# Kernel tuning notes

Measured on AMD Instinct MI355X. Metric: run time of the kernel, lower is better.

## Reference

```python
import jax, jax.numpy as jnp
import numpy as np

NUM_PQ = 8
TAU_Q = 1.0
EPS = 1e-12


def setup_inputs() -> dict:
    key = jax.random.key(0)
    k1, k2 = jax.random.split(key)
    z = jax.random.normal(k1, (8, 384, 32, 32), dtype=jnp.float32)
    # xavier_uniform bound for [2048, 384] is ~0.0497; approximate scale with normal init
    C = jax.random.normal(k2, (2048, 384), dtype=jnp.float32) * 0.05
    return {"z": z, "C": C, "it": 0}


def _soft_pq(z, C):
    b, c, h, w = z.shape
    K = NUM_PQ
    d = c // K
    # flatten spatial -> [N, K, d] sub-vectors (torch.split along channel == reshape)
    x = z.transpose(0, 2, 3, 1).reshape(-1, K, d)          # [N, K, d]
    cb = C.reshape(-1, K, d)                               # [M, K, d]
    x2 = jnp.sum(x * x, axis=-1)[:, :, None]               # [N, K, 1]
    c2 = jnp.sum(cb * cb, axis=-1).T[None, :, :]           # [1, K, M]
    xc = jnp.einsum('nkd,mkd->nkm', x, cb)                 # [N, K, M]
    dist = x2 + c2 - 2.0 * xc                              # [N, K, M]
    soft = jax.nn.softmax(-TAU_Q * dist, axis=-1)          # per-book softmax over M
    # soft assignment -> weighted codeword sum, concat over books
    Zq = jnp.einsum('nkm,mkd->nkd', soft, cb).reshape(-1, c)
    # JSD between first/second halves of the batch, per book, averaged over books
    N = soft.shape[0]
    p, q = soft[: N // 2], soft[N // 2 :]
    m = 0.5 * (p + q)
    logm = jnp.log(m + EPS)
    kl_pm = jnp.sum(p * (jnp.log(p + EPS) - logm), axis=-1)   # [N/2, K]
    kl_qm = jnp.sum(q * (jnp.log(q + EPS) - logm), axis=-1)
    # per-book JSD = mean over rows; sum over books / K == mean over both axes
    jsd = jnp.mean(0.5 * (kl_pm + kl_qm))
    z_quantized = Zq.reshape(b, h, w, c).transpose(0, 3, 1, 2)
    return z_quantized, jsd


def reference(z, C, it):
    z_quantized, jsd = _soft_pq(z, C)
    return z_quantized, jsd
```

## Files before the change

### kernel.cpp

```cpp
#include <hip/hip_runtime.h>


typedef __attribute__((ext_vector_type(8))) short short8;
typedef __attribute__((ext_vector_type(4))) float f32x4;

#define Z_BCH   (384*1024)
#define JSD_IDX 3145728
#define CS_TILE 9216
#define CT_TILE 6912
#define CT_OFF  (8*32*CS_TILE)

__device__ __forceinline__ f32x4 mfma32(short8 a, short8 b, f32x4 c) {
    return __builtin_amdgcn_mfma_f32_16x16x32_bf16(a, b, c, 0, 0, 0);
}
__device__ __forceinline__ unsigned short f2bf(float x) {
    unsigned u = __float_as_uint(x);
    u += 0x7FFF + ((u >> 16) & 1);
    return (unsigned short)(u >> 16);
}
__device__ __forceinline__ unsigned pk2bf(float a, float b) {
    return (unsigned)f2bf(a) | ((unsigned)f2bf(b) << 16);
}
__device__ __forceinline__ float bf2f(unsigned short h) {
    return __uint_as_float(((unsigned)h) << 16);
}

__global__ __launch_bounds__(256)
void pq_prep(const float* __restrict__ Cb, unsigned char* __restrict__ ws)
{
    const int tid = threadIdx.x;
    const int k   = blockIdx.x >> 5;
    const int t   = blockIdx.x & 31;
    const int sm  = tid & 63, p8 = tid >> 6;
    const int m   = t*64 + sm;

    unsigned short* csT = (unsigned short*)(ws + (size_t)(k*32 + t)*CS_TILE);
    unsigned short* ctT = (unsigned short*)(ws + CT_OFF + (size_t)(k*32 + t)*CT_TILE);

    const float4* crow = (const float4*)(Cb + (size_t)m*384 + k*48);
    float4 va = crow[p8*3+0], vb = crow[p8*3+1], vc = crow[p8*3+2];
    const int d0 = p8*12;
    *(uint2*)(csT + sm*72 + d0 + 0) = make_uint2(pk2bf(va.x,va.y), pk2bf(va.z,va.w));
    *(uint2*)(csT + sm*72 + d0 + 4) = make_uint2(pk2bf(vb.x,vb.y), pk2bf(vb.z,vb.w));
    *(uint2*)(csT + sm*72 + d0 + 8) = make_uint2(pk2bf(vc.x,vc.y), pk2bf(vc.z,vc.w));
    ctT[(d0+ 0)*72+sm] = f2bf(va.x);  ctT[(d0+ 1)*72+sm] = f2bf(va.y);
    ctT[(d0+ 2)*72+sm] = f2bf(va.z);  ctT[(d0+ 3)*72+sm] = f2bf(va.w);
    ctT[(d0+ 4)*72+sm] = f2bf(vb.x);  ctT[(d0+ 5)*72+sm] = f2bf(vb.y);
    ctT[(d0+ 6)*72+sm] = f2bf(vb.z);  ctT[(d0+ 7)*72+sm] = f2bf(vb.w);
    ctT[(d0+ 8)*72+sm] = f2bf(vc.x);  ctT[(d0+ 9)*72+sm] = f2bf(vc.y);
    ctT[(d0+10)*72+sm] = f2bf(vc.z);  ctT[(d0+11)*72+sm] = f2bf(vc.w);
    if (tid < 64) {
        const float4* cr2 = (const float4*)(Cb + (size_t)(t*64 + tid)*384 + k*48);
        float c2 = 0.f;
#pragma unroll
        for (int i = 0; i < 12; ++i) {
            float4 v = cr2[i];
            c2 += v.x*v.x + v.y*v.y + v.z*v.z + v.w*v.w;
        }
        float mh = -0.5f*c2;
        unsigned short hi = f2bf(mh);
        unsigned short lo = f2bf(mh - bf2f(hi));
        *(uint2*)(csT + tid*72 + 48) = make_uint2((unsigned)hi | ((unsigned)lo << 16), 0u);
        *(uint2*)(csT + tid*72 + 52) = make_uint2(0u, 0u);
        *(uint2*)(csT + tid*72 + 56) = make_uint2(0u, 0u);
        *(uint2*)(csT + tid*72 + 60) = make_uint2(0u, 0u);
    }
}

__global__ __launch_bounds__(512, 4)
void pq_pc(const float* __restrict__ Zin, const unsigned char* __restrict__ ws,
           float* __restrict__ Out)
{
    __shared__ __align__(16) unsigned char smem[54816];
    unsigned short* cs  = (unsigned short*)smem;
    unsigned short* ctb = (unsigned short*)(smem + 18432);
    unsigned short* xs  = (unsigned short*)smem;
    float* ztP  = (float*)(smem + 52736);
    float* ttP  = (float*)(smem + 52992);
    float* ztQ  = (float*)(smem + 53248);
    float* ttQ  = (float*)(smem + 53504);
    float* ipzP = (float*)(smem + 53760);
    float* ipzQ = (float*)(smem + 54016);
    float* entP = (float*)(smem + 54272);
    float* entQ = (float*)(smem + 54528);
    float* misc = (float*)(smem + 54784);
    float* obuf = (float*)smem;

    const int tid  = threadIdx.x;
    const int lane = tid & 63;
    const int wv   = tid >> 6;
    const int rg   = wv & 3;
    const int chw  = wv >> 2;
    const int lr   = lane & 15;
    const int lg   = lane >> 4;
    const int pg   = blockIdx.x & 63;
    const int k    = blockIdx.x >> 6;

    unsigned short* plds = (unsigned short*)(smem + 32256 + wv*2560);
    const unsigned char* csg = ws + (size_t)(k*32)*CS_TILE;
    const unsigned char* ctg = ws + CT_OFF + (size_t)(k*32)*CT_TILE;

    short8 av, on;
#pragma unroll
    for (int i = 0; i < 8; ++i) { av[i] = (short)f2bf((float)lr); on[i] = (short)0x3F80; }
    f32x4 zf4 = {0.f,0.f,0.f,0.f};
    f32x4 dmv = mfma32(av, on, zf4);
    f32x4 drv = mfma32(on, av, zf4);
    int mS[4], rS[4];
#pragma unroll
    for (int j = 0; j < 4; ++j) {
        mS[j] = ((int)(dmv[j]*0.03125f + 0.5f)) & 15;
        rS[j] = ((int)(drv[j]*0.03125f + 0.5f)) & 15;
    }
    const bool packOK = __all(mS[1] == mS[0]+1 && mS[2] == mS[0]+2 && mS[3] == mS[0]+3
                              && rS[1] == rS[0] && rS[2] == rS[0] && rS[3] == rS[0]);

    for (int i = tid; i < 4608; i += 512) ((unsigned*)smem)[i] = 0u;
    if (tid < 256) ((float*)(smem + 52736))[tid] = 0.f;
    __syncthreads();
    for (int i = tid; i < 6144; i += 512) {
        int row = i & 127, d = i >> 7;
        int n = pg*64 + (row & 63) + ((row & 64) ? 4096 : 0);
        xs[row*72 + d] = f2bf(Zin[(size_t)(n >> 10)*Z_BCH + (k*48 + d)*1024 + (n & 1023)]);
    }
    if (tid < 128) { xs[tid*72 + 48] = 0x3F80; xs[tid*72 + 49] = 0x3F80; }
    __syncthreads();
    short8 xf[2][2];
#pragma unroll
    for (int kh = 0; kh < 2; ++kh) {
        xf[0][kh] = *(const short8*)(xs + (rg*16 + lr)*72 + kh*32 + lg*8);
        xf[1][kh] = *(const short8*)(xs + (64 + rg*16 + lr)*72 + kh*32 + lg*8);
    }
    __syncthreads();

    uint4 r0, r1, r2;
#define LOADREG(t, doCT) do {                                                 \
        const unsigned char* _c = csg + (size_t)(t)*CS_TILE;                  \
        r0 = *(const uint4*)(_c + tid*16);                                    \
        if (tid < 64) r1 = *(const uint4*)(_c + 8192 + tid*16);               \
        if ((doCT) && tid < 432)                                              \
            r2 = *(const uint4*)(ctg + (size_t)(t)*CT_TILE + tid*16);         \
    } while (0)

#define SWRITE(b, doCT) do {                                                  \
        *(uint4*)(smem + (b)*CS_TILE + tid*16) = r0;                          \
        if (tid < 64) *(uint4*)(smem + (b)*CS_TILE + 8192 + tid*16) = r1;     \
        if ((doCT) && tid < 432)                                              \
            *(uint4*)(smem + 18432 + (b)*CT_TILE + tid*16) = r2;              \
    } while (0)

    float zp[4]={0,0,0,0}, tp[4]={0,0,0,0}, zq[4]={0,0,0,0}, tq[4]={0,0,0,0};

    LOADREG(0, false);
    SWRITE(0, false);
    LOADREG(1, false);
    __syncthreads();

#pragma unroll 1
    for (int t = 0; t < 32; ++t) {
        if (t < 31) SWRITE((t+1)&1, false);
        if (t < 30) LOADREG(t+2, false);
        const unsigned short* cst = cs + (t&1)*4608;
#pragma unroll
        for (int lmt = 0; lmt < 2; ++lmt) {
            const int mt = chw*2 + lmt;
            short8 a0 = *(const short8*)(cst + (mt*16 + lr)*72 + lg*8);
            short8 a1 = *(const short8*)(cst + (mt*16 + lr)*72 + 32 + lg*8);
            f32x4 accP = {0.f,0.f,0.f,0.f}, accQ = {0.f,0.f,0.f,0.f};
            accP = mfma32(a0, xf[0][0], accP);
            accP = mfma32(a1, xf[0][1], accP);
            accQ = mfma32(a0, xf[1][0], accQ);
            accQ = mfma32(a1, xf[1][1], accQ);
#pragma unroll
            for (int j = 0; j < 4; ++j) {
                float sp = 2.f*accP[j], sq = 2.f*accQ[j];
                float e1 = __expf(sp), e2 = __expf(sq);
                zp[j] += e1; tp[j] = fmaf(e1, sp, tp[j]);
                zq[j] += e2; tq[j] = fmaf(e2, sq, tq[j]);
            }
        }
        __syncthreads();
    }

#pragma unroll
    for (int j = 0; j < 4; ++j) {
        int r = rg*16 + rS[j];
        atomicAdd(ztP + r, zp[j]); atomicAdd(ttP + r, tp[j]);
        atomicAdd(ztQ + r, zq[j]); atomicAdd(ttQ + r, tq[j]);
    }
    __syncthreads();
    if (tid < 64) {
        float z1 = ztP[tid], t1 = ttP[tid];
        float z2 = ztQ[tid], t2 = ttQ[tid];
        float i1 = 1.f/z1, i2 = 1.f/z2;
        ipzP[tid] = i1; entP[tid] = t1*i1 - __logf(z1);
        ipzQ[tid] = i2; entQ[tid] = t2*i2 - __logf(z2);
    }
    __syncthreads();
    float izp_s[4], izq_s[4];
#pragma unroll
    for (int j = 0; j < 4; ++j) {
        izp_s[j] = ipzP[rg*16 + rS[j]];
        izq_s[j] = ipzQ[rg*16 + rS[j]];
    }

    f32x4 Op[3], Oq[3];
#pragma unroll
    for (int dt = 0; dt < 3; ++dt) { Op[dt] = (f32x4){0.f,0.f,0.f,0.f}; Oq[dt] = (f32x4){0.f,0.f,0.f,0.f}; }
    float cross = 0.f;

    LOADREG(0, true);
    SWRITE(0, true);
    LOADREG(1, true);
    __syncthreads();

#pragma unroll 1
    for (int t = 0; t < 32; ++t) {
        if (t < 31) SWRITE((t+1)&1, true);
        if (t < 30) LOADREG(t+2, true);
        const unsigned short* cst = cs + (t&1)*4608;
        const unsigned short* ctt = ctb + (t&1)*3456;
#pragma unroll
        for (int lmt = 0; lmt < 2; ++lmt) {
            const int mt = chw*2 + lmt;
            short8 a0 = *(const short8*)(cst + (mt*16 + lr)*72 + lg*8);
            short8 a1 = *(const short8*)(cst + (mt*16 + lr)*72 + 32 + lg*8);
            f32x4 accP = {0.f,0.f,0.f,0.f}, accQ = {0.f,0.f,0.f,0.f};
            accP = mfma32(a0, xf[0][0], accP);
            accP = mfma32(a1, xf[0][1], accP);
            accQ = mfma32(a0, xf[1][0], accQ);
            accQ = mfma32(a1, xf[1][1], accQ);
            float e1a[4], e2a[4];
#pragma unroll
            for (int j = 0; j < 4; ++j) {
                float e1 = __expf(2.f*accP[j]);
                float e2 = __expf(2.f*accQ[j]);
                e1a[j] = e1; e2a[j] = e2;
                float p = e1*izp_s[j], q = e2*izq_s[j];
                float ss = p + q;
                cross = fmaf(ss, __logf(fmaf(0.5f, ss, 1e-12f)), cross);
            }
            if (packOK) {
                *(uint2*)(plds + rS[0]*40        + lmt*16 + mS[0]) =
                    make_uint2(pk2bf(e1a[0], e1a[1]), pk2bf(e1a[2], e1a[3]));
                *(uint2*)(plds + (16 + rS[0])*40 + lmt*16 + mS[0]) =
                    make_uint2(pk2bf(e2a[0], e2a[1]), pk2bf(e2a[2], e2a[3]));
            } else {
#pragma unroll
                for (int j = 0; j < 4; ++j) {
                    plds[rS[j]*40        + lmt*16 + mS[j]] = f2bf(e1a[j]);
                    plds[(16 + rS[j])*40 + lmt*16 + mS[j]] = f2bf(e2a[j]);
                }
            }
        }
        {
            short8 pA = *(const short8*)(plds + lr*40        + lg*8);
            short8 qA = *(const short8*)(plds + (16 + lr)*40 + lg*8);
#pragma unroll
            for (int dt = 0; dt < 3; ++dt) {
                short8 cB = *(const short8*)(ctt + (dt*16 + lr)*72 + chw*32 + lg*8);
                Op[dt] = mfma32(pA, cB, Op[dt]);
                Oq[dt] = mfma32(qA, cB, Oq[dt]);
            }
        }
        __syncthreads();
    }

#pragma unroll
    for (int off = 1; off < 64; off <<= 1) cross += __shfl_xor(cross, off);
    if (lane == 0) misc[wv] = cross;

    if (chw == 1) {
#pragma unroll
        for (int dt = 0; dt < 3; ++dt)
#pragma unroll
            for (int j = 0; j < 4; ++j) {
                obuf[(rg*32 +      mS[j])*48 + dt*16 + rS[j]] = Op[dt][j];
                obuf[(rg*32 + 16 + mS[j])*48 + dt*16 + rS[j]] = Oq[dt][j];
            }
    }
    __syncthreads();

    if (tid == 0) {
        float es = 0.f;
        for (int r = 0; r < 64; ++r) es += entP[r] + entQ[r];
        float cr = 0.f;
        for (int w = 0; w < 8; ++w) cr += misc[w];
        atomicAdd(Out + JSD_IDX, (es - cr) * (0.5f/32768.f));
    }

    if (chw == 0) {
#pragma unroll
        for (int dt = 0; dt < 3; ++dt)
#pragma unroll
            for (int j = 0; j < 4; ++j) {
                int xr = mS[j];
                int np = pg*64 + rg*16 + xr;
                int nq = np + 4096;
                int chc = k*48 + dt*16 + rS[j];
                float vP = (Op[dt][j] + obuf[(rg*32 +      xr)*48 + dt*16 + rS[j]]) * ipzP[rg*16 + xr];
                float vQ = (Oq[dt][j] + obuf[(rg*32 + 16 + xr)*48 + dt*16 + rS[j]]) * ipzQ[rg*16 + xr];
                Out[(size_t)(np >> 10)*Z_BCH + (size_t)chc*1024 + (np & 1023)] = vP;
                Out[(size_t)(nq >> 10)*Z_BCH + (size_t)chc*1024 + (nq & 1023)] = vQ;
            }
    }
}

extern "C" void kernel_launch(void* const* d_in, const int* in_sizes, int n_in,
                              void* d_out, int out_size, void* d_ws, size_t ws_size,
                              hipStream_t stream)
{
    const float* z = (const float*)d_in[0];
    const float* C = (const float*)d_in[1];
    float* out = (float*)d_out;

    hipMemsetAsync(out + JSD_IDX, 0, sizeof(float), stream);

    pq_prep<<<dim3(256), dim3(256), 0, stream>>>(C, (unsigned char*)d_ws);
    pq_pc<<<dim3(512), dim3(512), 0, stream>>>(z, (const unsigned char*)d_ws, out);
}
```

Measured before the change: 146.6 us.

## Split fused PQ kernel into stats and output passes over halved codebook ranges

The single fused kernel is split into two kernels, pq_stats and pq_out, and each block now covers half of the codebook tiles. This doubles the grid from 512 to 1024 blocks for more parallelism. Row partition sums are combined through global atomics into a workspace, and the output is accumulated with atomicAdd, which requires zeroing the whole output buffer beforehand. The exponentials switch to exp2f/log2f with prescaled constants, and the codeword-transpose tile is read straight from global memory instead of being staged in LDS. In exchange it adds an extra launch, two memsets, recomputation of the x fragments and distances, and many float atomics on the output.

```diff
diff --git a/kernel.cpp b/kernel.cpp
--- a/kernel.cpp
+++ b/kernel.cpp
@@ -8,7 +8,11 @@
 #define JSD_IDX 3145728
 #define CS_TILE 9216
 #define CT_TILE 6912
-#define CT_OFF  (8*32*CS_TILE)
+#define CT_OFF  2359296
+#define ZS_OFF  4128768
+#define TS_OFF  (ZS_OFF + 262144)
+#define KC      2.8853900817779268f
+#define LN2     0.6931471805599453f
 
 __device__ __forceinline__ f32x4 mfma32(short8 a, short8 b, f32x4 c) {
     return __builtin_amdgcn_mfma_f32_16x16x32_bf16(a, b, c, 0, 0, 0);
@@ -67,100 +71,92 @@
     }
 }
 
-__global__ __launch_bounds__(512, 4)
-void pq_pc(const float* __restrict__ Zin, const unsigned char* __restrict__ ws,
-           float* __restrict__ Out)
-{
-    __shared__ __align__(16) unsigned char smem[54816];
-    unsigned short* cs  = (unsigned short*)smem;
-    unsigned short* ctb = (unsigned short*)(smem + 18432);
-    unsigned short* xs  = (unsigned short*)smem;
-    float* ztP  = (float*)(smem + 52736);
-    float* ttP  = (float*)(smem + 52992);
-    float* ztQ  = (float*)(smem + 53248);
-    float* ttQ  = (float*)(smem + 53504);
-    float* ipzP = (float*)(smem + 53760);
-    float* ipzQ = (float*)(smem + 54016);
-    float* entP = (float*)(smem + 54272);
-    float* entQ = (float*)(smem + 54528);
-    float* misc = (float*)(smem + 54784);
-    float* obuf = (float*)smem;
-
-    const int tid  = threadIdx.x;
-    const int lane = tid & 63;
-    const int wv   = tid >> 6;
-    const int rg   = wv & 3;
-    const int chw  = wv >> 2;
-    const int lr   = lane & 15;
-    const int lg   = lane >> 4;
-    const int pg   = blockIdx.x & 63;
-    const int k    = blockIdx.x >> 6;
-
-    unsigned short* plds = (unsigned short*)(smem + 32256 + wv*2560);
-    const unsigned char* csg = ws + (size_t)(k*32)*CS_TILE;
-    const unsigned char* ctg = ws + CT_OFF + (size_t)(k*32)*CT_TILE;
-
-    short8 av, on;
-#pragma unroll
-    for (int i = 0; i < 8; ++i) { av[i] = (short)f2bf((float)lr); on[i] = (short)0x3F80; }
-    f32x4 zf4 = {0.f,0.f,0.f,0.f};
-    f32x4 dmv = mfma32(av, on, zf4);
-    f32x4 drv = mfma32(on, av, zf4);
-    int mS[4], rS[4];
-#pragma unroll
-    for (int j = 0; j < 4; ++j) {
-        mS[j] = ((int)(dmv[j]*0.03125f + 0.5f)) & 15;
-        rS[j] = ((int)(drv[j]*0.03125f + 0.5f)) & 15;
-    }
-    const bool packOK = __all(mS[1] == mS[0]+1 && mS[2] == mS[0]+2 && mS[3] == mS[0]+3
-                              && rS[1] == rS[0] && rS[2] == rS[0] && rS[3] == rS[0]);
-
-    for (int i = tid; i < 4608; i += 512) ((unsigned*)smem)[i] = 0u;
-    if (tid < 256) ((float*)(smem + 52736))[tid] = 0.f;
-    __syncthreads();
-    for (int i = tid; i < 6144; i += 512) {
-        int row = i & 127, d = i >> 7;
-        int n = pg*64 + (row & 63) + ((row & 64) ? 4096 : 0);
-        xs[row*72 + d] = f2bf(Zin[(size_t)(n >> 10)*Z_BCH + (k*48 + d)*1024 + (n & 1023)]);
-    }
-    if (tid < 128) { xs[tid*72 + 48] = 0x3F80; xs[tid*72 + 49] = 0x3F80; }
-    __syncthreads();
-    short8 xf[2][2];
-#pragma unroll
-    for (int kh = 0; kh < 2; ++kh) {
-        xf[0][kh] = *(const short8*)(xs + (rg*16 + lr)*72 + kh*32 + lg*8);
-        xf[1][kh] = *(const short8*)(xs + (64 + rg*16 + lr)*72 + kh*32 + lg*8);
-    }
-    __syncthreads();
-
-    uint4 r0, r1, r2;
-#define LOADREG(t, doCT) do {                                                 \
+#define PQ_DECODE                                                             \
+    const int tid  = threadIdx.x;                                             \
+    const int lane = tid & 63;                                                \
+    const int wv   = tid >> 6;                                                \
+    const int rg   = wv & 3;                                                  \
+    const int chw  = wv >> 2;                                                 \
+    const int lr   = lane & 15;                                               \
+    const int lg   = lane >> 4;                                               \
+    const int pg   = blockIdx.x & 63;                                         \
+    const int half = (blockIdx.x >> 6) & 1;                                   \
+    const int k    = blockIdx.x >> 7;                                         \
+    const int t0   = half*16;
+
+#define PQ_PROBES                                                             \
+    short8 av, on;                                                            \
+    _Pragma("unroll")                                                         \
+    for (int i = 0; i < 8; ++i) { av[i] = (short)f2bf((float)lr); on[i] = (short)0x3F80; } \
+    f32x4 zf4 = {0.f,0.f,0.f,0.f};                                            \
+    f32x4 dmv = mfma32(av, on, zf4);                                          \
+    f32x4 drv = mfma32(on, av, zf4);                                          \
+    int mS[4], rS[4];                                                         \
+    _Pragma("unroll")                                                         \
+    for (int j = 0; j < 4; ++j) {                                             \
+        mS[j] = ((int)(dmv[j]*0.03125f + 0.5f)) & 15;                         \
+        rS[j] = ((int)(drv[j]*0.03125f + 0.5f)) & 15;                         \
+    }
+
+#define PQ_XFRAGS(Zin)                                                        \
+    for (int i = tid; i < 6144; i += 512) {                                   \
+        int row = i & 127, d = i >> 7;                                        \
+        int n = pg*64 + (row & 63) + ((row & 64) ? 4096 : 0);                 \
+        xs[row*72 + d] = f2bf(Zin[(size_t)(n >> 10)*Z_BCH + (k*48 + d)*1024 + (n & 1023)]); \
+    }                                                                         \
+    if (tid < 128) { xs[tid*72 + 48] = 0x3F80; xs[tid*72 + 49] = 0x3F80; }    \
+    __syncthreads();                                                          \
+    short8 xf[2][2];                                                          \
+    _Pragma("unroll")                                                         \
+    for (int kh = 0; kh < 2; ++kh) {                                          \
+        xf[0][kh] = *(const short8*)(xs + (rg*16 + lr)*72 + kh*32 + lg*8);    \
+        xf[1][kh] = *(const short8*)(xs + (64 + rg*16 + lr)*72 + kh*32 + lg*8); \
+    }                                                                         \
+    __syncthreads();
+
+#define LOADREG(t) do {                                                       \
         const unsigned char* _c = csg + (size_t)(t)*CS_TILE;                  \
         r0 = *(const uint4*)(_c + tid*16);                                    \
         if (tid < 64) r1 = *(const uint4*)(_c + 8192 + tid*16);               \
-        if ((doCT) && tid < 432)                                              \
-            r2 = *(const uint4*)(ctg + (size_t)(t)*CT_TILE + tid*16);         \
     } while (0)
-
-#define SWRITE(b, doCT) do {                                                  \
+#define SWRITE(b) do {                                                        \
         *(uint4*)(smem + (b)*CS_TILE + tid*16) = r0;                          \
         if (tid < 64) *(uint4*)(smem + (b)*CS_TILE + 8192 + tid*16) = r1;     \
-        if ((doCT) && tid < 432)                                              \
-            *(uint4*)(smem + 18432 + (b)*CT_TILE + tid*16) = r2;              \
     } while (0)
 
+__global__ __launch_bounds__(512, 8)
+void pq_stats(const float* __restrict__ Zin, const unsigned char* __restrict__ ws,
+              float* __restrict__ wsZ, float* __restrict__ wsT)
+{
+    __shared__ __align__(16) unsigned char smem[19456];
+    unsigned short* xs = (unsigned short*)smem;
+    float* ztP = (float*)(smem + 18432);
+    float* ttP = (float*)(smem + 18688);
+    float* ztQ = (float*)(smem + 18944);
+    float* ttQ = (float*)(smem + 19200);
+
+    PQ_DECODE
+    PQ_PROBES
+    const unsigned char* csg = ws + (size_t)(k*32)*CS_TILE;
+
+    for (int i = tid; i < 4608; i += 512) ((unsigned*)smem)[i] = 0u;
+    if (tid < 256) ((float*)(smem + 18432))[tid] = 0.f;
+    __syncthreads();
+    PQ_XFRAGS(Zin)
+
+    uint4 r0, r1;
     float zp[4]={0,0,0,0}, tp[4]={0,0,0,0}, zq[4]={0,0,0,0}, tq[4]={0,0,0,0};
 
-    LOADREG(0, false);
-    SWRITE(0, false);
-    LOADREG(1, false);
+    LOADREG(t0);
+    SWRITE(0);
+    LOADREG(t0+1);
     __syncthreads();
 
 #pragma unroll 1
-    for (int t = 0; t < 32; ++t) {
-        if (t < 31) SWRITE((t+1)&1, false);
-        if (t < 30) LOADREG(t+2, false);
-        const unsigned short* cst = cs + (t&1)*4608;
+    for (int t = 0; t < 16; ++t) {
+        if (t < 15) SWRITE((t+1)&1);
+        if (t < 14) LOADREG(t0+t+2);
+        const unsigned short* cst = (const unsigned short*)(smem + (t&1)*CS_TILE);
 #pragma unroll
         for (int lmt = 0; lmt < 2; ++lmt) {
             const int mt = chw*2 + lmt;
@@ -173,10 +169,10 @@
             accQ = mfma32(a1, xf[1][1], accQ);
 #pragma unroll
             for (int j = 0; j < 4; ++j) {
-                float sp = 2.f*accP[j], sq = 2.f*accQ[j];
-                float e1 = __expf(sp), e2 = __expf(sq);
-                zp[j] += e1; tp[j] = fmaf(e1, sp, tp[j]);
-                zq[j] += e2; tq[j] = fmaf(e2, sq, tq[j]);
+                float s2p = accP[j]*KC, s2q = accQ[j]*KC;
+                float e1 = exp2f(s2p), e2 = exp2f(s2q);
+                zp[j] += e1; tp[j] = fmaf(e1, s2p, tp[j]);
+                zq[j] += e2; tq[j] = fmaf(e2, s2q, tq[j]);
             }
         }
         __syncthreads();
@@ -189,37 +185,75 @@
         atomicAdd(ztQ + r, zq[j]); atomicAdd(ttQ + r, tq[j]);
     }
     __syncthreads();
-    if (tid < 64) {
-        float z1 = ztP[tid], t1 = ttP[tid];
-        float z2 = ztQ[tid], t2 = ttQ[tid];
-        float i1 = 1.f/z1, i2 = 1.f/z2;
-        ipzP[tid] = i1; entP[tid] = t1*i1 - __logf(z1);
-        ipzQ[tid] = i2; entQ[tid] = t2*i2 - __logf(z2);
+    if (tid < 128) {
+        int r = tid & 63;
+        int n = pg*64 + r + ((tid & 64) ? 4096 : 0);
+        float zv = (tid < 64) ? ztP[r] : ztQ[r];
+        float tv = (tid < 64) ? ttP[r] : ttQ[r];
+        atomicAdd(wsZ + (k << 13) + n, zv);
+        atomicAdd(wsT + (k << 13) + n, tv);
+    }
+}
+
+__global__ __launch_bounds__(512, 6)
+void pq_out(const float* __restrict__ Zin, const unsigned char* __restrict__ ws,
+            const float* __restrict__ wsZ, const float* __restrict__ wsT,
+            float* __restrict__ Out)
+{
+    __shared__ __align__(16) unsigned char smem[39968];
+    unsigned short* xs = (unsigned short*)smem;
+    float* ipz  = (float*)(smem + 38912);
+    float* ent  = (float*)(smem + 39424);
+    float* misc = (float*)(smem + 39936);
+    float* obuf = (float*)smem;
+
+    PQ_DECODE
+    PQ_PROBES
+    const bool packOK = __all(mS[1] == mS[0]+1 && mS[2] == mS[0]+2 && mS[3] == mS[0]+3
+                              && rS[1] == rS[0] && rS[2] == rS[0] && rS[3] == rS[0]);
+    const unsigned char* csg = ws + (size_t)(k*32)*CS_TILE;
+    const unsigned char* ctg = ws + CT_OFF + (size_t)(k*32)*CT_TILE;
+    unsigned short* plds = (unsigned short*)(smem + 18432 + wv*2560);
+
+    for (int i = tid; i < 4608; i += 512) ((unsigned*)smem)[i] = 0u;
+    __syncthreads();
+    PQ_XFRAGS(Zin)
+    if (tid < 128) {
+        int n = pg*64 + (tid & 63) + ((tid & 64) ? 4096 : 0);
+        float Zr = wsZ[(k << 13) + n];
+        float Tr = wsT[(k << 13) + n];
+        float iz = 1.f / Zr;
+        ipz[tid] = iz;
+        ent[tid] = LN2*(Tr*iz) - __logf(Zr);
     }
     __syncthreads();
     float izp_s[4], izq_s[4];
 #pragma unroll
     for (int j = 0; j < 4; ++j) {
-        izp_s[j] = ipzP[rg*16 + rS[j]];
-        izq_s[j] = ipzQ[rg*16 + rS[j]];
-    }
-
+        izp_s[j] = ipz[rg*16 + rS[j]];
+        izq_s[j] = ipz[64 + rg*16 + rS[j]];
+    }
+
+    uint4 r0, r1;
     f32x4 Op[3], Oq[3];
 #pragma unroll
     for (int dt = 0; dt < 3; ++dt) { Op[dt] = (f32x4){0.f,0.f,0.f,0.f}; Oq[dt] = (f32x4){0.f,0.f,0.f,0.f}; }
-    float cross = 0.f;
-
-    LOADREG(0, true);
-    SWRITE(0, true);
-    LOADREG(1, true);
+    float cross2 = 0.f;
+
+    LOADREG(t0);
+    SWRITE(0);
+    LOADREG(t0+1);
     __syncthreads();
 
 #pragma unroll 1
-    for (int t = 0; t < 32; ++t) {
-        if (t < 31) SWRITE((t+1)&1, true);
-        if (t < 30) LOADREG(t+2, true);
-        const unsigned short* cst = cs + (t&1)*4608;
-        const unsigned short* ctt = ctb + (t&1)*3456;
+    for (int t = 0; t < 16; ++t) {
+        if (t < 15) SWRITE((t+1)&1);
+        if (t < 14) LOADREG(t0+t+2);
+        const unsigned short* ctt = (const unsigned short*)(ctg + (size_t)(t0+t)*CT_TILE);
+        short8 cB0 = *(const short8*)(ctt + (     lr)*72 + chw*32 + lg*8);
+        short8 cB1 = *(const short8*)(ctt + (16 + lr)*72 + chw*32 + lg*8);
+        short8 cB2 = *(const short8*)(ctt + (32 + lr)*72 + chw*32 + lg*8);
+        const unsigned short* cst = (const unsigned short*)(smem + (t&1)*CS_TILE);
 #pragma unroll
         for (int lmt = 0; lmt < 2; ++lmt) {
             const int mt = chw*2 + lmt;
@@ -233,12 +267,11 @@
             float e1a[4], e2a[4];
 #pragma unroll
             for (int j = 0; j < 4; ++j) {
-                float e1 = __expf(2.f*accP[j]);
-                float e2 = __expf(2.f*accQ[j]);
+                float e1 = exp2f(accP[j]*KC);
+                float e2 = exp2f(accQ[j]*KC);
                 e1a[j] = e1; e2a[j] = e2;
-                float p = e1*izp_s[j], q = e2*izq_s[j];
-                float ss = p + q;
-                cross = fmaf(ss, __logf(fmaf(0.5f, ss, 1e-12f)), cross);
+                float ss = fmaf(e1, izp_s[j], e2*izq_s[j]);
+                cross2 = fmaf(ss, log2f(fmaf(0.5f, ss, 1e-12f)), cross2);
             }
             if (packOK) {
                 *(uint2*)(plds + rS[0]*40        + lmt*16 + mS[0]) =
@@ -256,19 +289,19 @@
         {
             short8 pA = *(const short8*)(plds + lr*40        + lg*8);
             short8 qA = *(const short8*)(plds + (16 + lr)*40 + lg*8);
-#pragma unroll
-            for (int dt = 0; dt < 3; ++dt) {
-                short8 cB = *(const short8*)(ctt + (dt*16 + lr)*72 + chw*32 + lg*8);
-                Op[dt] = mfma32(pA, cB, Op[dt]);
-                Oq[dt] = mfma32(qA, cB, Oq[dt]);
-            }
+            Op[0] = mfma32(pA, cB0, Op[0]);
+            Oq[0] = mfma32(qA, cB0, Oq[0]);
+            Op[1] = mfma32(pA, cB1, Op[1]);
+            Oq[1] = mfma32(qA, cB1, Oq[1]);
+            Op[2] = mfma32(pA, cB2, Op[2]);
+            Oq[2] = mfma32(qA, cB2, Oq[2]);
         }
         __syncthreads();
     }
 
 #pragma unroll
-    for (int off = 1; off < 64; off <<= 1) cross += __shfl_xor(cross, off);
-    if (lane == 0) misc[wv] = cross;
+    for (int off = 1; off < 64; off <<= 1) cross2 += __shfl_xor(cross2, off);
+    if (lane == 0) misc[wv] = cross2;
 
     if (chw == 1) {
 #pragma unroll
@@ -282,11 +315,15 @@
     __syncthreads();
 
     if (tid == 0) {
-        float es = 0.f;
-        for (int r = 0; r < 64; ++r) es += entP[r] + entQ[r];
         float cr = 0.f;
         for (int w = 0; w < 8; ++w) cr += misc[w];
-        atomicAdd(Out + JSD_IDX, (es - cr) * (0.5f/32768.f));
+        float val = -LN2 * cr;
+        if (half == 0) {
+            float es = 0.f;
+            for (int r = 0; r < 128; ++r) es += ent[r];
+            val += es;
+        }
+        atomicAdd(Out + JSD_IDX, val * (0.5f/32768.f));
     }
 
     if (chw == 0) {
@@ -298,10 +335,10 @@
                 int np = pg*64 + rg*16 + xr;
                 int nq = np + 4096;
                 int chc = k*48 + dt*16 + rS[j];
-                float vP = (Op[dt][j] + obuf[(rg*32 +      xr)*48 + dt*16 + rS[j]]) * ipzP[rg*16 + xr];
-                float vQ = (Oq[dt][j] + obuf[(rg*32 + 16 + xr)*48 + dt*16 + rS[j]]) * ipzQ[rg*16 + xr];
-                Out[(size_t)(np >> 10)*Z_BCH + (size_t)chc*1024 + (np & 1023)] = vP;
-                Out[(size_t)(nq >> 10)*Z_BCH + (size_t)chc*1024 + (nq & 1023)] = vQ;
+                float vP = (Op[dt][j] + obuf[(rg*32 +      xr)*48 + dt*16 + rS[j]]) * ipz[rg*16 + xr];
+                float vQ = (Oq[dt][j] + obuf[(rg*32 + 16 + xr)*48 + dt*16 + rS[j]]) * ipz[64 + rg*16 + xr];
+                atomicAdd(Out + (size_t)(np >> 10)*Z_BCH + (size_t)chc*1024 + (np & 1023), vP);
+                atomicAdd(Out + (size_t)(nq >> 10)*Z_BCH + (size_t)chc*1024 + (nq & 1023), vQ);
             }
     }
 }
@@ -313,9 +350,14 @@
     const float* z = (const float*)d_in[0];
     const float* C = (const float*)d_in[1];
     float* out = (float*)d_out;
-
-    hipMemsetAsync(out + JSD_IDX, 0, sizeof(float), stream);
-
-    pq_prep<<<dim3(256), dim3(256), 0, stream>>>(C, (unsigned char*)d_ws);
-    pq_pc<<<dim3(512), dim3(512), 0, stream>>>(z, (const unsigned char*)d_ws, out);
-}
+    unsigned char* ws = (unsigned char*)d_ws;
+    float* wsZ = (float*)(ws + ZS_OFF);
+    float* wsT = (float*)(ws + TS_OFF);
+
+    hipMemsetAsync(out, 0, (size_t)out_size*4, stream);
+    hipMemsetAsync(ws + ZS_OFF, 0, 524288, stream);
+
+    pq_prep <<<dim3(256),  dim3(256), 0, stream>>>(C, ws);
+    pq_stats<<<dim3(1024), dim3(512), 0, stream>>>(z, ws, wsZ, wsT);
+    pq_out  <<<dim3(1024), dim3(512), 0, stream>>>(z, ws, wsZ, wsT, out);
+}
```

New measurement: 375.0 us. 2.56x slower.

## Halve rows per block and split P·C work across waves with double-buffered P tiles

Applied to the files above, without the earlier changes.

Each block now handles 32 rows per half instead of 64, so the grid doubles to 1024 blocks, and each wave owns one codeword m-tile instead of two. In the second pass the per-wave P/Q staging buffers are double-buffered and shared across waves: each wave computes either the P or the Q output against one half of the codeword chunk, which removes a barrier per iteration. This is meant to give more parallelism and shorter per-wave dependency chains. In exchange the codebook tiles are loaded twice as many times overall, raising global/L2 traffic.

```diff
diff --git a/kernel.cpp b/kernel.cpp
--- a/kernel.cpp
+++ b/kernel.cpp
@@ -8,7 +8,7 @@
 #define JSD_IDX 3145728
 #define CS_TILE 9216
 #define CT_TILE 6912
-#define CT_OFF  (8*32*CS_TILE)
+#define CT_OFF  2359296
 
 __device__ __forceinline__ f32x4 mfma32(short8 a, short8 b, f32x4 c) {
     return __builtin_amdgcn_mfma_f32_16x16x32_bf16(a, b, c, 0, 0, 0);
@@ -68,37 +68,32 @@
 }
 
 __global__ __launch_bounds__(512, 4)
-void pq_pc(const float* __restrict__ Zin, const unsigned char* __restrict__ ws,
-           float* __restrict__ Out)
+void pq_f(const float* __restrict__ Zin, const unsigned char* __restrict__ ws,
+          float* __restrict__ Out)
 {
-    __shared__ __align__(16) unsigned char smem[54816];
-    unsigned short* cs  = (unsigned short*)smem;
-    unsigned short* ctb = (unsigned short*)(smem + 18432);
-    unsigned short* xs  = (unsigned short*)smem;
-    float* ztP  = (float*)(smem + 52736);
-    float* ttP  = (float*)(smem + 52992);
-    float* ztQ  = (float*)(smem + 53248);
-    float* ttQ  = (float*)(smem + 53504);
-    float* ipzP = (float*)(smem + 53760);
-    float* ipzQ = (float*)(smem + 54016);
-    float* entP = (float*)(smem + 54272);
-    float* entQ = (float*)(smem + 54528);
-    float* misc = (float*)(smem + 54784);
+    __shared__ __align__(16) unsigned char smem[53280];
+    unsigned short* xs = (unsigned short*)smem;
+    float* ztP  = (float*)(smem + 32256);
+    float* ttP  = (float*)(smem + 32384);
+    float* ztQ  = (float*)(smem + 32512);
+    float* ttQ  = (float*)(smem + 32640);
+    float* ipz  = (float*)(smem + 52736);
+    float* ent  = (float*)(smem + 52992);
+    float* misc = (float*)(smem + 53248);
     float* obuf = (float*)smem;
 
     const int tid  = threadIdx.x;
     const int lane = tid & 63;
     const int wv   = tid >> 6;
-    const int rg   = wv & 3;
-    const int chw  = wv >> 2;
+    const int rg   = wv & 1;
+    const int ch2  = wv >> 1;
+    const int lmt  = ch2 & 1;
+    const int pgrp = ch2 >> 1;
+    const int role = ch2 & 1;
     const int lr   = lane & 15;
     const int lg   = lane >> 4;
-    const int pg   = blockIdx.x & 63;
-    const int k    = blockIdx.x >> 6;
-
-    unsigned short* plds = (unsigned short*)(smem + 32256 + wv*2560);
-    const unsigned char* csg = ws + (size_t)(k*32)*CS_TILE;
-    const unsigned char* ctg = ws + CT_OFF + (size_t)(k*32)*CT_TILE;
+    const int pg   = blockIdx.x & 127;
+    const int k    = blockIdx.x >> 7;
 
     short8 av, on;
 #pragma unroll
@@ -115,69 +110,71 @@
     const bool packOK = __all(mS[1] == mS[0]+1 && mS[2] == mS[0]+2 && mS[3] == mS[0]+3
                               && rS[1] == rS[0] && rS[2] == rS[0] && rS[3] == rS[0]);
 
-    for (int i = tid; i < 4608; i += 512) ((unsigned*)smem)[i] = 0u;
-    if (tid < 256) ((float*)(smem + 52736))[tid] = 0.f;
-    __syncthreads();
-    for (int i = tid; i < 6144; i += 512) {
-        int row = i & 127, d = i >> 7;
-        int n = pg*64 + (row & 63) + ((row & 64) ? 4096 : 0);
+    const unsigned char* csg = ws + (size_t)(k*32)*CS_TILE;
+    const unsigned char* ctg = ws + CT_OFF + (size_t)(k*32)*CT_TILE;
+
+    for (int i = tid; i < 2304; i += 512) ((unsigned*)smem)[i] = 0u;
+    if (tid < 128) ((float*)(smem + 32256))[tid] = 0.f;
+    __syncthreads();
+    for (int i = tid; i < 3072; i += 512) {
+        int row = i & 63, d = i >> 6;
+        int n = pg*32 + (row & 31) + ((row & 32) ? 4096 : 0);
         xs[row*72 + d] = f2bf(Zin[(size_t)(n >> 10)*Z_BCH + (k*48 + d)*1024 + (n & 1023)]);
     }
-    if (tid < 128) { xs[tid*72 + 48] = 0x3F80; xs[tid*72 + 49] = 0x3F80; }
+    if (tid < 64) { xs[tid*72 + 48] = 0x3F80; xs[tid*72 + 49] = 0x3F80; }
     __syncthreads();
     short8 xf[2][2];
 #pragma unroll
     for (int kh = 0; kh < 2; ++kh) {
         xf[0][kh] = *(const short8*)(xs + (rg*16 + lr)*72 + kh*32 + lg*8);
-        xf[1][kh] = *(const short8*)(xs + (64 + rg*16 + lr)*72 + kh*32 + lg*8);
+        xf[1][kh] = *(const short8*)(xs + (32 + rg*16 + lr)*72 + kh*32 + lg*8);
     }
     __syncthreads();
 
     uint4 r0, r1, r2;
-#define LOADREG(t, doCT) do {                                                 \
+#define LOADREG(t) do {                                                       \
         const unsigned char* _c = csg + (size_t)(t)*CS_TILE;                  \
         r0 = *(const uint4*)(_c + tid*16);                                    \
         if (tid < 64) r1 = *(const uint4*)(_c + 8192 + tid*16);               \
-        if ((doCT) && tid < 432)                                              \
-            r2 = *(const uint4*)(ctg + (size_t)(t)*CT_TILE + tid*16);         \
     } while (0)
-
-#define SWRITE(b, doCT) do {                                                  \
+#define SWRITE(b) do {                                                        \
         *(uint4*)(smem + (b)*CS_TILE + tid*16) = r0;                          \
         if (tid < 64) *(uint4*)(smem + (b)*CS_TILE + 8192 + tid*16) = r1;     \
-        if ((doCT) && tid < 432)                                              \
-            *(uint4*)(smem + 18432 + (b)*CT_TILE + tid*16) = r2;              \
     } while (0)
+#define LOADREG_CT(t) do {                                                    \
+        LOADREG(t);                                                           \
+        if (tid < 432) r2 = *(const uint4*)(ctg + (size_t)(t)*CT_TILE + tid*16); \
+    } while (0)
+#define SWRITE_CT(b) do {                                                     \
+        SWRITE(b);                                                            \
+        if (tid < 432) *(uint4*)(smem + 18432 + (b)*CT_TILE + tid*16) = r2;   \
+    } while (0)
 
     float zp[4]={0,0,0,0}, tp[4]={0,0,0,0}, zq[4]={0,0,0,0}, tq[4]={0,0,0,0};
 
-    LOADREG(0, false);
-    SWRITE(0, false);
-    LOADREG(1, false);
+    LOADREG(0);
+    SWRITE(0);
+    LOADREG(1);
     __syncthreads();
 
 #pragma unroll 1
     for (int t = 0; t < 32; ++t) {
-        if (t < 31) SWRITE((t+1)&1, false);
-        if (t < 30) LOADREG(t+2, false);
-        const unsigned short* cst = cs + (t&1)*4608;
-#pragma unroll
-        for (int lmt = 0; lmt < 2; ++lmt) {
-            const int mt = chw*2 + lmt;
-            short8 a0 = *(const short8*)(cst + (mt*16 + lr)*72 + lg*8);
-            short8 a1 = *(const short8*)(cst + (mt*16 + lr)*72 + 32 + lg*8);
-            f32x4 accP = {0.f,0.f,0.f,0.f}, accQ = {0.f,0.f,0.f,0.f};
-            accP = mfma32(a0, xf[0][0], accP);
-            accP = mfma32(a1, xf[0][1], accP);
-            accQ = mfma32(a0, xf[1][0], accQ);
-            accQ = mfma32(a1, xf[1][1], accQ);
-#pragma unroll
-            for (int j = 0; j < 4; ++j) {
-                float sp = 2.f*accP[j], sq = 2.f*accQ[j];
-                float e1 = __expf(sp), e2 = __expf(sq);
-                zp[j] += e1; tp[j] = fmaf(e1, sp, tp[j]);
-                zq[j] += e2; tq[j] = fmaf(e2, sq, tq[j]);
-            }
+        if (t < 31) SWRITE((t+1)&1);
+        if (t < 30) LOADREG(t+2);
+        const unsigned short* cst = (const unsigned short*)(smem + (t&1)*CS_TILE);
+        short8 a0 = *(const short8*)(cst + (ch2*16 + lr)*72 + lg*8);
+        short8 a1 = *(const short8*)(cst + (ch2*16 + lr)*72 + 32 + lg*8);
+        f32x4 accP = {0.f,0.f,0.f,0.f}, accQ = {0.f,0.f,0.f,0.f};
+        accP = mfma32(a0, xf[0][0], accP);
+        accP = mfma32(a1, xf[0][1], accP);
+        accQ = mfma32(a0, xf[1][0], accQ);
+        accQ = mfma32(a1, xf[1][1], accQ);
+#pragma unroll
+        for (int j = 0; j < 4; ++j) {
+            float sp = 2.f*accP[j], sq = 2.f*accQ[j];
+            float e1 = __expf(sp), e2 = __expf(sq);
+            zp[j] += e1; tp[j] = fmaf(e1, sp, tp[j]);
+            zq[j] += e2; tq[j] = fmaf(e2, sq, tq[j]);
         }
         __syncthreads();
     }
@@ -190,118 +187,113 @@
     }
     __syncthreads();
     if (tid < 64) {
-        float z1 = ztP[tid], t1 = ttP[tid];
-        float z2 = ztQ[tid], t2 = ttQ[tid];
-        float i1 = 1.f/z1, i2 = 1.f/z2;
-        ipzP[tid] = i1; entP[tid] = t1*i1 - __logf(z1);
-        ipzQ[tid] = i2; entQ[tid] = t2*i2 - __logf(z2);
+        int r = tid & 31;
+        float z1 = (tid < 32) ? ztP[r] : ztQ[r];
+        float t1 = (tid < 32) ? ttP[r] : ttQ[r];
+        float i1 = 1.f/z1;
+        ipz[tid] = i1;
+        ent[tid] = t1*i1 - __logf(z1);
     }
     __syncthreads();
     float izp_s[4], izq_s[4];
 #pragma unroll
     for (int j = 0; j < 4; ++j) {
-        izp_s[j] = ipzP[rg*16 + rS[j]];
-        izq_s[j] = ipzQ[rg*16 + rS[j]];
-    }
-
-    f32x4 Op[3], Oq[3];
-#pragma unroll
-    for (int dt = 0; dt < 3; ++dt) { Op[dt] = (f32x4){0.f,0.f,0.f,0.f}; Oq[dt] = (f32x4){0.f,0.f,0.f,0.f}; }
+        izp_s[j] = ipz[rg*16 + rS[j]];
+        izq_s[j] = ipz[32 + rg*16 + rS[j]];
+    }
+
+    f32x4 Oa[3];
+#pragma unroll
+    for (int dt = 0; dt < 3; ++dt) Oa[dt] = (f32x4){0.f,0.f,0.f,0.f};
     float cross = 0.f;
 
-    LOADREG(0, true);
-    SWRITE(0, true);
-    LOADREG(1, true);
+    LOADREG_CT(0);
+    SWRITE_CT(0);
+    LOADREG_CT(1);
     __syncthreads();
 
 #pragma unroll 1
     for (int t = 0; t < 32; ++t) {
-        if (t < 31) SWRITE((t+1)&1, true);
-        if (t < 30) LOADREG(t+2, true);
-        const unsigned short* cst = cs + (t&1)*4608;
-        const unsigned short* ctt = ctb + (t&1)*3456;
-#pragma unroll
-        for (int lmt = 0; lmt < 2; ++lmt) {
-            const int mt = chw*2 + lmt;
-            short8 a0 = *(const short8*)(cst + (mt*16 + lr)*72 + lg*8);
-            short8 a1 = *(const short8*)(cst + (mt*16 + lr)*72 + 32 + lg*8);
-            f32x4 accP = {0.f,0.f,0.f,0.f}, accQ = {0.f,0.f,0.f,0.f};
-            accP = mfma32(a0, xf[0][0], accP);
-            accP = mfma32(a1, xf[0][1], accP);
-            accQ = mfma32(a0, xf[1][0], accQ);
-            accQ = mfma32(a1, xf[1][1], accQ);
-            float e1a[4], e2a[4];
+        if (t < 31) SWRITE_CT((t+1)&1);
+        if (t < 30) LOADREG_CT(t+2);
+        const unsigned short* cst = (const unsigned short*)(smem + (t&1)*CS_TILE);
+        const unsigned short* ctt = (const unsigned short*)(smem + 18432 + (t&1)*CT_TILE);
+        unsigned short* pw = (unsigned short*)(smem + 32256 + ((t&1)*4 + rg*2 + pgrp)*2560);
+
+        short8 a0 = *(const short8*)(cst + (ch2*16 + lr)*72 + lg*8);
+        short8 a1 = *(const short8*)(cst + (ch2*16 + lr)*72 + 32 + lg*8);
+        f32x4 accP = {0.f,0.f,0.f,0.f}, accQ = {0.f,0.f,0.f,0.f};
+        accP = mfma32(a0, xf[0][0], accP);
+        accP = mfma32(a1, xf[0][1], accP);
+        accQ = mfma32(a0, xf[1][0], accQ);
+        accQ = mfma32(a1, xf[1][1], accQ);
+        float e1a[4], e2a[4];
+#pragma unroll
+        for (int j = 0; j < 4; ++j) {
+            float e1 = __expf(2.f*accP[j]);
+            float e2 = __expf(2.f*accQ[j]);
+            e1a[j] = e1; e2a[j] = e2;
+            float ss = fmaf(e1, izp_s[j], e2*izq_s[j]);
+            cross = fmaf(ss, __logf(fmaf(0.5f, ss, 1e-12f)), cross);
+        }
+        if (packOK) {
+            *(uint2*)(pw + rS[0]*40        + lmt*16 + mS[0]) =
+                make_uint2(pk2bf(e1a[0], e1a[1]), pk2bf(e1a[2], e1a[3]));
+            *(uint2*)(pw + (16 + rS[0])*40 + lmt*16 + mS[0]) =
+                make_uint2(pk2bf(e2a[0], e2a[1]), pk2bf(e2a[2], e2a[3]));
+        } else {
 #pragma unroll
             for (int j = 0; j < 4; ++j) {
-                float e1 = __expf(2.f*accP[j]);
-                float e2 = __expf(2.f*accQ[j]);
-                e1a[j] = e1; e2a[j] = e2;
-                float p = e1*izp_s[j], q = e2*izq_s[j];
-                float ss = p + q;
-                cross = fmaf(ss, __logf(fmaf(0.5f, ss, 1e-12f)), cross);
+                pw[rS[j]*40        + lmt*16 + mS[j]] = f2bf(e1a[j]);
+                pw[(16 + rS[j])*40 + lmt*16 + mS[j]] = f2bf(e2a[j]);
             }
-            if (packOK) {
-                *(uint2*)(plds + rS[0]*40        + lmt*16 + mS[0]) =
-                    make_uint2(pk2bf(e1a[0], e1a[1]), pk2bf(e1a[2], e1a[3]));
-                *(uint2*)(plds + (16 + rS[0])*40 + lmt*16 + mS[0]) =
-                    make_uint2(pk2bf(e2a[0], e2a[1]), pk2bf(e2a[2], e2a[3]));
-            } else {
-#pragma unroll
-                for (int j = 0; j < 4; ++j) {
-                    plds[rS[j]*40        + lmt*16 + mS[j]] = f2bf(e1a[j]);
-                    plds[(16 + rS[j])*40 + lmt*16 + mS[j]] = f2bf(e2a[j]);
-                }
-            }
-        }
+        }
+        short8 cB0 = *(const short8*)(ctt + (     lr)*72 + pgrp*32 + lg*8);
+        short8 cB1 = *(const short8*)(ctt + (16 + lr)*72 + pgrp*32 + lg*8);
+        short8 cB2 = *(const short8*)(ctt + (32 + lr)*72 + pgrp*32 + lg*8);
+        __syncthreads();
         {
-            short8 pA = *(const short8*)(plds + lr*40        + lg*8);
-            short8 qA = *(const short8*)(plds + (16 + lr)*40 + lg*8);
-#pragma unroll
-            for (int dt = 0; dt < 3; ++dt) {
-                short8 cB = *(const short8*)(ctt + (dt*16 + lr)*72 + chw*32 + lg*8);
-                Op[dt] = mfma32(pA, cB, Op[dt]);
-                Oq[dt] = mfma32(qA, cB, Oq[dt]);
-            }
-        }
-        __syncthreads();
+            const unsigned short* pA = pw + (role ? 16 : 0)*40;
+            short8 pAv = *(const short8*)(pA + lr*40 + lg*8);
+            Oa[0] = mfma32(pAv, cB0, Oa[0]);
+            Oa[1] = mfma32(pAv, cB1, Oa[1]);
+            Oa[2] = mfma32(pAv, cB2, Oa[2]);
+        }
     }
 
 #pragma unroll
     for (int off = 1; off < 64; off <<= 1) cross += __shfl_xor(cross, off);
     if (lane == 0) misc[wv] = cross;
-
-    if (chw == 1) {
+    __syncthreads();
+
+    if (pgrp == 1) {
 #pragma unroll
         for (int dt = 0; dt < 3; ++dt)
 #pragma unroll
-            for (int j = 0; j < 4; ++j) {
-                obuf[(rg*32 +      mS[j])*48 + dt*16 + rS[j]] = Op[dt][j];
-                obuf[(rg*32 + 16 + mS[j])*48 + dt*16 + rS[j]] = Oq[dt][j];
-            }
+            for (int j = 0; j < 4; ++j)
+                obuf[((rg*2 + role)*16 + mS[j])*48 + dt*16 + rS[j]] = Oa[dt][j];
     }
     __syncthreads();
 
     if (tid == 0) {
         float es = 0.f;
-        for (int r = 0; r < 64; ++r) es += entP[r] + entQ[r];
+        for (int r = 0; r < 64; ++r) es += ent[r];
         float cr = 0.f;
         for (int w = 0; w < 8; ++w) cr += misc[w];
         atomicAdd(Out + JSD_IDX, (es - cr) * (0.5f/32768.f));
     }
 
-    if (chw == 0) {
+    if (pgrp == 0) {
 #pragma unroll
         for (int dt = 0; dt < 3; ++dt)
 #pragma unroll
             for (int j = 0; j < 4; ++j) {
                 int xr = mS[j];
-                int np = pg*64 + rg*16 + xr;
-                int nq = np + 4096;
+                int n = pg*32 + rg*16 + xr + (role ? 4096 : 0);
                 int chc = k*48 + dt*16 + rS[j];
-                float vP = (Op[dt][j] + obuf[(rg*32 +      xr)*48 + dt*16 + rS[j]]) * ipzP[rg*16 + xr];
-                float vQ = (Oq[dt][j] + obuf[(rg*32 + 16 + xr)*48 + dt*16 + rS[j]]) * ipzQ[rg*16 + xr];
-                Out[(size_t)(np >> 10)*Z_BCH + (size_t)chc*1024 + (np & 1023)] = vP;
-                Out[(size_t)(nq >> 10)*Z_BCH + (size_t)chc*1024 + (nq & 1023)] = vQ;
+                float v = (Oa[dt][j] + obuf[((rg*2 + role)*16 + xr)*48 + dt*16 + rS[j]])
+                          * ipz[role*32 + rg*16 + xr];
+                Out[(size_t)(n >> 10)*Z_BCH + (size_t)chc*1024 + (n & 1023)] = v;
             }
     }
 }
@@ -313,9 +305,10 @@
     const float* z = (const float*)d_in[0];
     const float* C = (const float*)d_in[1];
     float* out = (float*)d_out;
+    unsigned char* ws = (unsigned char*)d_ws;
 
     hipMemsetAsync(out + JSD_IDX, 0, sizeof(float), stream);
 
-    pq_prep<<<dim3(256), dim3(256), 0, stream>>>(C, (unsigned char*)d_ws);
-    pq_pc<<<dim3(512), dim3(512), 0, stream>>>(z, (const unsigned char*)d_ws, out);
-}
+    pq_prep<<<dim3(256),  dim3(256), 0, stream>>>(C, ws);
+    pq_f   <<<dim3(1024), dim3(512), 0, stream>>>(z, ws, out);
+}
```

New measurement: 184.0 us. 1.26x slower.
